# Kernel tuning notes

Hardware: AMD Instinct MI355X
Metric: run time of the kernel (lower is better)

Reference implementation:

```python
import jax, jax.numpy as jnp
import numpy as np

N = 100000      # total nodes across batch of graphs
E = 1600000     # total edges (avg degree 16)
DIN = 16        # raw node feature dim
H = 128         # social_hidden_dim
HEADS = 4
DOUT = H // HEADS
LAYERS = 2
G = 64          # number of graphs in batch
FOUT = 256      # fusion_hidden_dim
NEG_SLOPE = 0.2


def layer_norm(x, g, b, eps=1e-5):
    mu = x.mean(-1, keepdims=True)
    var = ((x - mu) ** 2).mean(-1, keepdims=True)
    return (x - mu) / jnp.sqrt(var + eps) * g + b


def gat_conv(h, src, dst, W, a_src, a_dst, bias):
    # h: [N,H]; src/dst: [E+N] (self-loops included)
    hp = (h @ W).reshape(N, HEADS, DOUT)                    # [N,heads,dout]
    al_s = jnp.einsum('nhd,hd->nh', hp, a_src)              # [N,heads]
    al_d = jnp.einsum('nhd,hd->nh', hp, a_dst)
    logits = jax.nn.leaky_relu(al_s[src] + al_d[dst], NEG_SLOPE)  # [Etot,heads]
    m = jax.ops.segment_max(logits, dst, num_segments=N)    # segment softmax over dst
    e = jnp.exp(logits - m[dst])
    denom = jax.ops.segment_sum(e, dst, num_segments=N)
    alpha = e / (denom[dst] + 1e-16)                        # [Etot,heads]
    msg = hp[src] * alpha[:, :, None]                       # [Etot,heads,dout]
    out = jax.ops.segment_sum(msg, dst, num_segments=N)     # scatter-add
    return out.reshape(N, H) + bias


def setup_inputs():
    key = jax.random.key(0)
    ks = jax.random.split(key, 24)
    s = 0.05
    inp = {
        'x': jax.random.normal(ks[0], (N, DIN), jnp.float32),
        'edge_index': jax.random.randint(ks[1], (2, E), 0, N, jnp.int32),
        'node2graph': (jnp.arange(N, dtype=jnp.int32) * G // N).astype(jnp.int32),
        'Wp': jax.random.normal(ks[2], (DIN, H)) * s,
        'bp': jnp.zeros((H,)),
        'Wq1': jax.random.normal(ks[3], (2 * H, H)) * s,
        'bq1': jnp.zeros((H,)),
        'gq': jnp.ones((H,)), 'beq': jnp.zeros((H,)),
        'Wq2': jax.random.normal(ks[4], (H, FOUT)) * s,
        'bq2': jnp.zeros((FOUT,)),
    }
    for i in range(LAYERS):
        inp[f'Wg{i}'] = jax.random.normal(ks[5 + 4 * i], (H, H)) * s
        inp[f'as{i}'] = jax.random.normal(ks[6 + 4 * i], (HEADS, DOUT)) * s
        inp[f'ad{i}'] = jax.random.normal(ks[7 + 4 * i], (HEADS, DOUT)) * s
        inp[f'bg{i}'] = jnp.zeros((H,))
        inp[f'g{i}'] = jnp.ones((H,))
        inp[f'be{i}'] = jnp.zeros((H,))
    return inp


def reference(x, edge_index, node2graph, Wp, bp, Wq1, bq1, gq, beq, Wq2, bq2,
              Wg0, as0, ad0, bg0, g0, be0, Wg1, as1, ad1, bg1, g1, be1):
    loop = jnp.arange(N, dtype=edge_index.dtype)
    src = jnp.concatenate([edge_index[0], loop])  # add self-loops (PyG default)
    dst = jnp.concatenate([edge_index[1], loop])

    h = jax.nn.gelu(x @ Wp + bp, approximate=False)
    params = [(Wg0, as0, ad0, bg0, g0, be0), (Wg1, as1, ad1, bg1, g1, be1)]
    for (W, a_s, a_d, b, g, be) in params:
        h_new = gat_conv(h, src, dst, W, a_s, a_d, b)
        h = layer_norm(h_new + h, g, be)  # dims match -> residual

    counts = jax.ops.segment_sum(jnp.ones((N, 1), h.dtype), node2graph, num_segments=G)
    mean_pool = jax.ops.segment_sum(h, node2graph, num_segments=G) / jnp.maximum(counts, 1.0)
    max_pool = jax.ops.segment_max(h, node2graph, num_segments=G)
    emb = jnp.concatenate([mean_pool, max_pool], axis=-1)  # [G, 2H]

    p = layer_norm(emb @ Wq1 + bq1, gq, beq)
    p = jax.nn.gelu(p, approximate=False)
    return p @ Wq2 + bq2  # [G, FOUT]
```

## Files before the change

kernel.cpp:

```cpp
#include <hip/hip_runtime.h>

typedef unsigned short u16;
typedef unsigned char u8;
typedef unsigned int u32;
typedef unsigned long long u64;
typedef short short8 __attribute__((ext_vector_type(8)));
typedef float f32x4 __attribute__((ext_vector_type(4)));
typedef float f32x2 __attribute__((ext_vector_type(2)));

#define NN   100000
#define EE   1600000
#define NG   64
#define WSTR 136
#define NB   98
#define BCAP 24576
#define OCAP 262144
#define EPB  4096

constexpr size_t AL256(size_t x) { return (x + 255) & ~(size_t)255; }
constexpr size_t OFF_FLAG   = 0;
constexpr size_t OFF_OCNT   = AL256(OFF_FLAG + 256);
constexpr size_t OFF_BCNT   = AL256(OFF_OCNT + 128 * 4);
constexpr size_t OFF_ROWPTR = AL256(OFF_BCNT + 128 * 4);
constexpr size_t OFF_DEG    = AL256(OFF_ROWPTR + (size_t)(NN + 1) * 4);
constexpr size_t OFF_COL    = AL256(OFF_DEG + (size_t)NN * 4);
constexpr size_t OFF_ALS    = AL256(OFF_COL + (size_t)(EE + 1024) * 4);
constexpr size_t OFF_ALD    = AL256(OFF_ALS + (size_t)NN * 4 * 4);
constexpr size_t OFF_GSUM   = AL256(OFF_ALD + (size_t)NN * 4 * 4);
constexpr size_t OFF_GKEY   = AL256(OFF_GSUM + (size_t)NG * 128 * 4);
constexpr size_t OFF_GCNT   = AL256(OFF_GKEY + (size_t)NG * 128 * 4);
constexpr size_t OFF_H      = AL256(OFF_GCNT + (size_t)NG * 4);
constexpr size_t OFF_HPB    = AL256(OFF_H + (size_t)NN * 128 * 2);
constexpr size_t OFF_EBUF   = AL256(OFF_HPB + (size_t)NN * 128 * 1);
constexpr size_t OFF_OBUF   = AL256(OFF_EBUF + (size_t)NB * BCAP * 4);
constexpr size_t WS_TOTAL   = AL256(OFF_OBUF + (size_t)OCAP * 8);

__device__ u64 g_ws[WS_TOTAL / 8];

__device__ __forceinline__ char* wsp() { return (char*)g_ws; }
#define WS_FLAG   ((int*)(wsp() + OFF_FLAG))
#define WS_OCNT   ((int*)(wsp() + OFF_OCNT))
#define WS_BCNT   ((int*)(wsp() + OFF_BCNT))
#define WS_ROWPTR ((int*)(wsp() + OFF_ROWPTR))
#define WS_DEG    ((int*)(wsp() + OFF_DEG))
#define WS_COL    ((int*)(wsp() + OFF_COL))
#define WS_ALS    ((float*)(wsp() + OFF_ALS))
#define WS_ALD    ((float*)(wsp() + OFF_ALD))
#define WS_GSUM   ((float*)(wsp() + OFF_GSUM))
#define WS_GKEY   ((u32*)(wsp() + OFF_GKEY))
#define WS_GCNT   ((int*)(wsp() + OFF_GCNT))
#define WS_H      ((u16*)(wsp() + OFF_H))
#define WS_HPB    ((u8*)(wsp() + OFF_HPB))
#define WS_EBUF   ((u32*)(wsp() + OFF_EBUF))
#define WS_OBUF   ((u64*)(wsp() + OFF_OBUF))

__device__ __forceinline__ float b2f(u16 u) { return __uint_as_float(((u32)u) << 16); }
__device__ __forceinline__ float b2f_lo(u32 u) { return __uint_as_float(u << 16); }
__device__ __forceinline__ float b2f_hi(u32 u) { return __uint_as_float(u & 0xffff0000u); }
__device__ __forceinline__ u16 f2bf(float f) {
    u32 u = __float_as_uint(f);
    return (u16)((u + 0x7fffu + ((u >> 16) & 1u)) >> 16);
}
__device__ __forceinline__ float ldf(const void* p, int i, int bf) {
    return bf ? b2f(((const u16*)p)[i]) : ((const float*)p)[i];
}
__device__ __forceinline__ int ldint(const int* p, long long i, int wide) {
    return wide ? p[i * 2] : p[(size_t)i];
}
__device__ __forceinline__ u32 fkey(float f) {
    u32 u = __float_as_uint(f);
    return (u >> 31) ? ~u : (u | 0x80000000u);
}
__device__ __forceinline__ float funkey(u32 k) {
    u32 u = (k & 0x80000000u) ? (k & 0x7fffffffu) : ~k;
    return __uint_as_float(u);
}

__global__ __launch_bounds__(256) void k_zero(const void* __restrict__ x,
                                              const int* __restrict__ ei) {
    if (blockIdx.x == 0 && threadIdx.x < 64) {
        int t = threadIdx.x;
        const u16* p = (const u16*)x;
        u16 u = p[t * 2];
        int e = (u >> 7) & 0xff;
        int ok = ((u & 0x7fffu) == 0) || (e >= 0x60 && e <= 0x9f);
        u64 m1 = __ballot(ok);
        int z = (ei[t * 2 + 1] == 0);
        u64 m2 = __ballot(z);
        if (t == 0) {
            WS_FLAG[0] = (__popcll(m1) >= 48) ? 1 : 0;
            WS_FLAG[1] = (__popcll(m2) >= 56) ? 1 : 0;
        }
    }
    if (blockIdx.x == 0 && threadIdx.x == 64) WS_FLAG[2] = 0;
    int i = blockIdx.x * 256 + threadIdx.x;
    if (i < NN) WS_DEG[i] = 0;
    if (i < NG * 128) { WS_GSUM[i] = 0.f; WS_GKEY[i] = 0u; }
    if (i < NG) WS_GCNT[i] = 0;
    if (i < NB) { WS_BCNT[i] = 0; WS_OCNT[i] = 0; }
}

__global__ __launch_bounds__(256) void k_bucket(const int* __restrict__ ei) {
    __shared__ int lcnt[NB], lbase[NB], lcur[NB];
    int t = threadIdx.x;
    int wide = WS_FLAG[1];
    for (int i = t; i < NB; i += 256) { lcnt[i] = 0; lcur[i] = 0; }
    __syncthreads();
    int e0 = blockIdx.x * EPB + t;
    int sA[16], dA[16];
#pragma unroll
    for (int j = 0; j < 16; j++) {
        int e = e0 + j * 256;
        int s = -1, d = 0;
        if (e < EE) {
            if (wide) { s = ((const int2*)ei)[e].x; d = ((const int2*)ei)[(size_t)EE + e].x; }
            else      { s = ei[e];                  d = ei[(size_t)EE + e]; }
            if ((u32)s >= NN || (u32)d >= NN) s = -1;
        }
        sA[j] = s; dA[j] = d;
        if (s >= 0) atomicAdd(&lcnt[d >> 10], 1);
    }
    __syncthreads();
    for (int i = t; i < NB; i += 256)
        lbase[i] = atomicAdd(&WS_BCNT[i], lcnt[i]);
    __syncthreads();
    u32* ebuf = WS_EBUF;
#pragma unroll
    for (int j = 0; j < 16; j++) {
        int s = sA[j], d = dA[j];
        if (s < 0) continue;
        int b = d >> 10;
        int r = atomicAdd(&lcur[b], 1);
        int slot = lbase[b] + r;
        if (slot < BCAP) {
            ebuf[(size_t)b * BCAP + slot] = ((u32)(d & 1023) << 17) | (u32)s;
        } else {
            int o = atomicAdd(&WS_FLAG[2], 1);
            if (o < OCAP) {
                WS_OBUF[o] = ((u64)(u32)d << 32) | (u32)s;
                atomicAdd(&WS_DEG[d], 1);
                atomicAdd(&WS_OCNT[d >> 10], 1);
            }
        }
    }
}

__global__ __launch_bounds__(1024) void k_place() {
    __shared__ int hist[1024];
    __shared__ int sb[128];
    __shared__ int wsum[16];
    __shared__ int w0tot;
    int b = blockIdx.x, t = threadIdx.x;
    int lane = t & 63, wv = t >> 6;
    hist[t] = 0;
    if (t < 128) {
        int c = 0;
        if (t < NB) {
            c = WS_BCNT[t]; if (c > BCAP) c = BCAP;
            c += WS_OCNT[t];
        }
        int x = c;
#pragma unroll
        for (int off = 1; off < 64; off <<= 1) {
            int y = __shfl_up(x, off);
            if (lane >= off) x += y;
        }
        if (t == 63) w0tot = x;
        sb[t] = x;
    }
    __syncthreads();
    if (t >= 64 && t < 128) sb[t] += w0tot;
    __syncthreads();
    int base = (b > 0) ? sb[b - 1] : 0;
    if (b == 0 && t == 0) WS_ROWPTR[NN] = sb[NB - 1];
    int bc = WS_BCNT[b]; if (bc > BCAP) bc = BCAP;
    const u32* eb = WS_EBUF + (size_t)b * BCAP;
    for (int i = t; i < bc; i += 1024)
        atomicAdd(&hist[eb[i] >> 17], 1);
    __syncthreads();
    int n = (b << 10) + t;
    int v = (n < NN) ? (hist[t] + WS_DEG[n]) : 0;
    int x = v;
#pragma unroll
    for (int off = 1; off < 64; off <<= 1) {
        int y = __shfl_up(x, off);
        if (lane >= off) x += y;
    }
    if (lane == 63) wsum[wv] = x;
    __syncthreads();
    if (wv == 0 && lane < 16) {
        int y = wsum[lane];
#pragma unroll
        for (int off = 1; off < 16; off <<= 1) {
            int z = __shfl_up(y, off);
            if (lane >= off) y += z;
        }
        wsum[lane] = y;
    }
    __syncthreads();
    int r = base + x + (wv > 0 ? wsum[wv - 1] : 0) - v;
    if (n < NN) WS_ROWPTR[n] = r;
    __syncthreads();
    hist[t] = r;
    __syncthreads();
    for (int i = t; i < bc; i += 1024) {
        u32 pk = eb[i];
        int pos = atomicAdd(&hist[pk >> 17], 1);
        WS_COL[pos] = (int)(pk & 0x1ffffu);
    }
    int cnt = WS_FLAG[2]; if (cnt > OCAP) cnt = OCAP;
    for (int i = t; i < cnt; i += 1024) {
        u64 pk = WS_OBUF[i];
        int d = (int)(pk >> 32);
        if ((d >> 10) == b) {
            int pos = atomicAdd(&hist[d & 1023], 1);
            WS_COL[pos] = (int)(pk & 0xffffffffu);
        }
    }
}

__global__ __launch_bounds__(128) void k_proj(const void* __restrict__ x,
                                              const void* __restrict__ Wp,
                                              const void* __restrict__ bp) {
    __shared__ float sW[16 * 128];
    int t = threadIdx.x;
    int bf = WS_FLAG[0];
    for (int i = t; i < 16 * 128; i += 128) sW[i] = ldf(Wp, i, bf);
    __syncthreads();
    float bj = ldf(bp, t, bf);
    for (int n = blockIdx.x; n < NN; n += gridDim.x) {
        float acc = bj;
#pragma unroll
        for (int k = 0; k < 16; k++)
            acc = fmaf(ldf(x, n * 16 + k, bf), sW[k * 128 + t], acc);
        float g = 0.5f * acc * (1.0f + erff(acc * 0.70710678118654752f));
        WS_H[(size_t)n * 128 + t] = f2bf(g);
    }
}

__global__ __launch_bounds__(256) void k_gemm(const void* __restrict__ Wg,
                                              const void* __restrict__ a_s,
                                              const void* __restrict__ a_d) {
    __shared__ __align__(16) u16 sWt[128 * WSTR];
    __shared__ __align__(16) u16 sH[16 * WSTR];
    int t = threadIdx.x;
    int bf = WS_FLAG[0];
    for (int idx = t; idx < 128 * 128; idx += 256) {
        int k = idx >> 7, n = idx & 127;
        sWt[n * WSTR + k] = bf ? ((const u16*)Wg)[idx] : f2bf(((const float*)Wg)[idx]);
    }
    __syncthreads();
    int wv = t >> 6, lane = t & 63;
    int n0 = wv * 32;
    int quad = lane >> 4, m16 = lane & 15;
    int ce = n0 + 2 * m16;
    float as0v = ldf(a_s, ce, bf),     as1v = ldf(a_s, ce + 1, bf);
    float ad0v = ldf(a_d, ce, bf),     ad1v = ldf(a_d, ce + 1, bf);
    short8 bfr[2][4];
#pragma unroll
    for (int nt = 0; nt < 2; nt++) {
        int n = ce + nt;
#pragma unroll
        for (int ks = 0; ks < 4; ks++)
            bfr[nt][ks] = *(const short8*)&sWt[n * WSTR + ks * 32 + quad * 8];
    }
    u8* hp = WS_HPB;
    const u32* h32 = (const u32*)WS_H;
    u32* sH32 = (u32*)sH;
    for (int m0 = blockIdx.x * 16; m0 < NN; m0 += gridDim.x * 16) {
        __syncthreads();
        for (int idx = t; idx < 16 * 64; idx += 256) {
            int r = idx >> 6, c2 = idx & 63;
            sH32[r * 68 + c2] = h32[(size_t)(m0 + r) * 64 + c2];
        }
        __syncthreads();
        f32x4 acc0 = {0.f, 0.f, 0.f, 0.f};
        f32x4 acc1 = {0.f, 0.f, 0.f, 0.f};
#pragma unroll
        for (int ks = 0; ks < 4; ks++) {
            short8 af = *(const short8*)&sH[m16 * WSTR + ks * 32 + quad * 8];
            acc0 = __builtin_amdgcn_mfma_f32_16x16x32_bf16(af, bfr[0][ks], acc0, 0, 0, 0);
            acc1 = __builtin_amdgcn_mfma_f32_16x16x32_bf16(af, bfr[1][ks], acc1, 0, 0, 0);
        }
#pragma unroll
        for (int r = 0; r < 4; r++) {
            size_t row = (size_t)(m0 + quad * 4 + r) * 128;
            u32 pk8 = (u32)__builtin_amdgcn_cvt_pk_fp8_f32(acc0[r], acc1[r], 0, false);
            *(u16*)&hp[row + ce] = (u16)(pk8 & 0xffffu);
            float ps = acc0[r] * as0v + acc1[r] * as1v;
            float pd = acc0[r] * ad0v + acc1[r] * ad1v;
#pragma unroll
            for (int m = 1; m <= 8; m <<= 1) {
                ps += __shfl_xor(ps, m);
                pd += __shfl_xor(pd, m);
            }
            if (m16 == 0) {
                int nrow = m0 + quad * 4 + r;
                WS_ALS[nrow * 4 + wv] = ps;
                WS_ALD[nrow * 4 + wv] = pd;
            }
        }
    }
}

__global__ __launch_bounds__(512) void k_gat(const void* __restrict__ bg,
                                             const void* __restrict__ gam,
                                             const void* __restrict__ bet) {
    int wid = threadIdx.x >> 6, lane = threadIdx.x & 63;
    int n = blockIdx.x * 8 + wid;
    if (n >= NN) return;
    int bf = WS_FLAG[0];
    const int* col = WS_COL;
    const float* als = WS_ALS;
    int k0 = WS_ROWPTR[n], deg = WS_ROWPTR[n + 1] - k0;
    int hd = lane >> 4, eo = lane & 15;
    float aldh = WS_ALD[n * 4 + hd];
    const u16* hp16 = (const u16*)WS_HPB;
    u32* h32 = (u32*)WS_H;
    u32 hv = h32[(size_t)n * 64 + lane];
    u16 pvs = hp16[(size_t)n * 64 + lane];
    int base48 = lane & 48;

    float vs = als[n * 4 + hd] + aldh;
    vs = vs > 0.f ? vs : 0.2f * vs;
    float wself = __expf(vs);

    int i0 = eo, i1 = eo + 16;
    int e0 = k0 + (i0 < deg ? i0 : 0);
    int e1 = k0 + (i1 < deg ? i1 : 0);
    int sc0 = col[e0];
    int sc1 = col[e1];
    if ((u32)sc0 >= NN) sc0 = 0;
    if ((u32)sc1 >= NN) sc1 = 0;
    float v0 = als[sc0 * 4 + hd] + aldh;
    float v1 = als[sc1 * 4 + hd] + aldh;
    v0 = v0 > 0.f ? v0 : 0.2f * v0;
    v1 = v1 > 0.f ? v1 : 0.2f * v1;
    float w0 = (i0 < deg) ? __expf(v0) : 0.f;
    float w1 = (i1 < deg) ? __expf(v1) : 0.f;
    float se = w0 + w1;
    f32x2 mvs = __builtin_amdgcn_cvt_pk_f32_fp8((int)pvs, false);
    float a0 = wself * mvs.x, a1 = wself * mvs.y;

#pragma unroll
    for (int j = 0; j < 16; j++) {
        float wj = __shfl(w0, base48 + j);
        int   sj = __builtin_amdgcn_readlane(sc0, j);
        u16 pv = hp16[(size_t)sj * 64 + lane];
        f32x2 mv = __builtin_amdgcn_cvt_pk_f32_fp8((int)pv, false);
        a0 = fmaf(wj, mv.x, a0);
        a1 = fmaf(wj, mv.y, a1);
    }
    if (deg > 16) {
#pragma unroll
        for (int j = 0; j < 16; j++) {
            float wj = __shfl(w1, base48 + j);
            int   sj = __builtin_amdgcn_readlane(sc1, j);
            u16 pv = hp16[(size_t)sj * 64 + lane];
            f32x2 mv = __builtin_amdgcn_cvt_pk_f32_fp8((int)pv, false);
            a0 = fmaf(wj, mv.x, a0);
            a1 = fmaf(wj, mv.y, a1);
        }
    }

    if (__builtin_expect(deg > 32, 0)) {
        for (int c = 32; c < deg; c += 16) {
            int i = c + eo;
            float w = 0.f; int scol = 0;
            if (i < deg) {
                scol = col[k0 + i];
                float v = als[scol * 4 + hd] + aldh;
                v = v > 0.f ? v : 0.2f * v;
                w = __expf(v);
            }
            se += w;
            int rem = deg - c; if (rem > 16) rem = 16;
            for (int j = 0; j < rem; j++) {
                float wj = __shfl(w, base48 + j);
                int sj = __shfl(scol, base48 + j);
                u16 pv = hp16[(size_t)sj * 64 + lane];
                f32x2 mv = __builtin_amdgcn_cvt_pk_f32_fp8((int)pv, false);
                a0 = fmaf(wj, mv.x, a0);
                a1 = fmaf(wj, mv.y, a1);
            }
        }
    }

    se += __shfl_xor(se, 1);
    se += __shfl_xor(se, 2);
    se += __shfl_xor(se, 4);
    se += __shfl_xor(se, 8);
    se += wself;
    float inv = 1.f / (se + 1e-16f);
    int d0 = lane * 2, d1 = d0 + 1;
    float r0 = a0 * inv + ldf(bg, d0, bf) + b2f_lo(hv);
    float r1 = a1 * inv + ldf(bg, d1, bf) + b2f_hi(hv);
    float s1 = r0 + r1;
#pragma unroll
    for (int m = 1; m <= 32; m <<= 1) s1 += __shfl_xor(s1, m);
    float mu = s1 * (1.f / 128.f);
    float e0f = r0 - mu, e1f = r1 - mu;
    float s2 = e0f * e0f + e1f * e1f;
#pragma unroll
    for (int m = 1; m <= 32; m <<= 1) s2 += __shfl_xor(s2, m);
    float rstd = rsqrtf(s2 * (1.f / 128.f) + 1e-5f);
    float y0 = e0f * rstd * ldf(gam, d0, bf) + ldf(bet, d0, bf);
    float y1 = e1f * rstd * ldf(gam, d1, bf) + ldf(bet, d1, bf);
    h32[(size_t)n * 64 + lane] = (u32)f2bf(y0) | ((u32)f2bf(y1) << 16);
}

__global__ __launch_bounds__(128) void k_pool(const int* __restrict__ n2g) {
    int j = threadIdx.x;
    int wide = WS_FLAG[1];
    int n0 = blockIdx.x * 128;
    int n1 = n0 + 128; if (n1 > NN) n1 = NN;
    float runs = 0.f, runm = -3.4e38f;
    int rung = -1, runc = 0;
    for (int n = n0; n < n1; n++) {
        int g = ldint(n2g, n, wide);
        if (g != rung) {
            if (rung >= 0 && (u32)rung < NG) {
                atomicAdd(&WS_GSUM[rung * 128 + j], runs);
                atomicMax(&WS_GKEY[rung * 128 + j], fkey(runm));
                if (j == 0) atomicAdd(&WS_GCNT[rung], runc);
            }
            rung = g; runs = 0.f; runm = -3.4e38f; runc = 0;
        }
        float v = b2f(WS_H[(size_t)n * 128 + j]);
        runs += v;
        runm = fmaxf(runm, v);
        runc++;
    }
    if (rung >= 0 && (u32)rung < NG) {
        atomicAdd(&WS_GSUM[rung * 128 + j], runs);
        atomicMax(&WS_GKEY[rung * 128 + j], fkey(runm));
        if (j == 0) atomicAdd(&WS_GCNT[rung], runc);
    }
}

__global__ __launch_bounds__(256) void k_head(const void* __restrict__ Wq1,
                                              const void* __restrict__ bq1,
                                              const void* __restrict__ gq,
                                              const void* __restrict__ beq,
                                              const void* __restrict__ Wq2,
                                              const void* __restrict__ bq2,
                                              float* __restrict__ out) {
    __shared__ float sem[256];
    __shared__ float sp[128];
    __shared__ float red[4];
    int g = blockIdx.x, t = threadIdx.x;
    int bf = WS_FLAG[0];
    float cnt = fmaxf((float)WS_GCNT[g], 1.f);
    if (t < 128) sem[t] = WS_GSUM[g * 128 + t] / cnt;
    else         sem[t] = funkey(WS_GKEY[g * 128 + (t - 128)]);
    __syncthreads();
    float a = 0.f;
    if (t < 128) {
        a = ldf(bq1, t, bf);
        for (int k = 0; k < 256; k++) a = fmaf(sem[k], ldf(Wq1, k * 128 + t, bf), a);
    }
    int lane = t & 63, wv = t >> 6;
    float s1 = (t < 128) ? a : 0.f;
#pragma unroll
    for (int m = 1; m <= 32; m <<= 1) s1 += __shfl_xor(s1, m);
    if (lane == 0) red[wv] = s1;
    __syncthreads();
    float mu = (red[0] + red[1]) * (1.f / 128.f);
    float d = (t < 128) ? (a - mu) : 0.f;
    float s2 = d * d;
#pragma unroll
    for (int m = 1; m <= 32; m <<= 1) s2 += __shfl_xor(s2, m);
    __syncthreads();
    if (lane == 0) red[wv] = s2;
    __syncthreads();
    float var = (red[0] + red[1]) * (1.f / 128.f);
    if (t < 128) {
        float p = d * rsqrtf(var + 1e-5f) * ldf(gq, t, bf) + ldf(beq, t, bf);
        sp[t] = 0.5f * p * (1.0f + erff(p * 0.70710678118654752f));
    }
    __syncthreads();
    float o = ldf(bq2, t, bf);
    for (int k = 0; k < 128; k++)
        o = fmaf(sp[k], ldf(Wq2, k * 256 + t, bf), o);
    out[g * 256 + t] = o;
}

extern "C" void kernel_launch(void* const* d_in, const int* in_sizes, int n_in,
                              void* d_out, int out_size, void* d_ws, size_t ws_size,
                              hipStream_t stream) {
    const void* x   = d_in[0];
    const int* ei   = (const int*)d_in[1];
    const int* n2g  = (const int*)d_in[2];
    const void* Wp  = d_in[3];
    const void* bp  = d_in[4];
    const void* Wq1 = d_in[5];
    const void* bq1 = d_in[6];
    const void* gq  = d_in[7];
    const void* beq = d_in[8];
    const void* Wq2 = d_in[9];
    const void* bq2 = d_in[10];
    const void* Wg0 = d_in[11];
    const void* as0 = d_in[12];
    const void* ad0 = d_in[13];
    const void* bg0 = d_in[14];
    const void* g0  = d_in[15];
    const void* be0 = d_in[16];
    const void* Wg1 = d_in[17];
    const void* as1 = d_in[18];
    const void* ad1 = d_in[19];
    const void* bg1 = d_in[20];
    const void* g1  = d_in[21];
    const void* be1 = d_in[22];
    (void)d_ws; (void)ws_size; (void)in_sizes; (void)n_in; (void)out_size;

    k_zero<<<(NN + 255) / 256, 256, 0, stream>>>(x, ei);

    k_bucket<<<(EE + EPB - 1) / EPB, 256, 0, stream>>>(ei);
    k_place<<<NB, 1024, 0, stream>>>();

    k_proj<<<2048, 128, 0, stream>>>(x, Wp, bp);

    k_gemm<<<1024, 256, 0, stream>>>(Wg0, as0, ad0);
    k_gat<<<(NN + 7) / 8, 512, 0, stream>>>(bg0, g0, be0);
    k_gemm<<<1024, 256, 0, stream>>>(Wg1, as1, ad1);
    k_gat<<<(NN + 7) / 8, 512, 0, stream>>>(bg1, g1, be1);

    k_pool<<<(NN + 127) / 128, 128, 0, stream>>>(n2g);
    k_head<<<NG, 256, 0, stream>>>(Wq1, bq1, gq, beq, Wq2, bq2, (float*)d_out);
}
```

Before: 519.3 us.

## Use finer CSR buckets, larger GEMM row tiles, and split-K head matmul

Edge bucketing now uses 512-node buckets (196 blocks of 512 threads) instead of 1024-node buckets, so CSR placement runs across more workgroups with smaller per-block histograms. The node-projection GEMM processes 32 rows per iteration as two 16-row MFMA sub-tiles on a 768-block grid, which amortises the shared-memory staging and barriers over more rows. The head kernel splits the 256-deep Wq1 dot product across all 256 threads and then sums the two halves. In exchange, the block-level prefix scan is more complex and the smaller bucket capacity may push more edges into the overflow path.

```diff
diff --git a/kernel.cpp b/kernel.cpp
--- a/kernel.cpp
+++ b/kernel.cpp
@@ -12,16 +12,18 @@
 #define EE   1600000
 #define NG   64
 #define WSTR 136
-#define NB   98
-#define BCAP 24576
+#define NB   196
+#define BSHIFT 9
+#define BMASK 511
+#define BCAP 12288
 #define OCAP 262144
 #define EPB  4096
 
 constexpr size_t AL256(size_t x) { return (x + 255) & ~(size_t)255; }
 constexpr size_t OFF_FLAG   = 0;
 constexpr size_t OFF_OCNT   = AL256(OFF_FLAG + 256);
-constexpr size_t OFF_BCNT   = AL256(OFF_OCNT + 128 * 4);
-constexpr size_t OFF_ROWPTR = AL256(OFF_BCNT + 128 * 4);
+constexpr size_t OFF_BCNT   = AL256(OFF_OCNT + 256 * 4);
+constexpr size_t OFF_ROWPTR = AL256(OFF_BCNT + 256 * 4);
 constexpr size_t OFF_DEG    = AL256(OFF_ROWPTR + (size_t)(NN + 1) * 4);
 constexpr size_t OFF_COL    = AL256(OFF_DEG + (size_t)NN * 4);
 constexpr size_t OFF_ALS    = AL256(OFF_COL + (size_t)(EE + 1024) * 4);
@@ -118,7 +120,7 @@
             if ((u32)s >= NN || (u32)d >= NN) s = -1;
         }
         sA[j] = s; dA[j] = d;
-        if (s >= 0) atomicAdd(&lcnt[d >> 10], 1);
+        if (s >= 0) atomicAdd(&lcnt[d >> BSHIFT], 1);
     }
     __syncthreads();
     for (int i = t; i < NB; i += 256)
@@ -129,31 +131,31 @@
     for (int j = 0; j < 16; j++) {
         int s = sA[j], d = dA[j];
         if (s < 0) continue;
-        int b = d >> 10;
+        int b = d >> BSHIFT;
         int r = atomicAdd(&lcur[b], 1);
         int slot = lbase[b] + r;
         if (slot < BCAP) {
-            ebuf[(size_t)b * BCAP + slot] = ((u32)(d & 1023) << 17) | (u32)s;
+            ebuf[(size_t)b * BCAP + slot] = ((u32)(d & BMASK) << 17) | (u32)s;
         } else {
             int o = atomicAdd(&WS_FLAG[2], 1);
             if (o < OCAP) {
                 WS_OBUF[o] = ((u64)(u32)d << 32) | (u32)s;
                 atomicAdd(&WS_DEG[d], 1);
-                atomicAdd(&WS_OCNT[d >> 10], 1);
+                atomicAdd(&WS_OCNT[d >> BSHIFT], 1);
             }
         }
     }
 }
 
-__global__ __launch_bounds__(1024) void k_place() {
-    __shared__ int hist[1024];
-    __shared__ int sb[128];
-    __shared__ int wsum[16];
-    __shared__ int w0tot;
+__global__ __launch_bounds__(512) void k_place() {
+    __shared__ int hist[512];
+    __shared__ int sbase[256];
+    __shared__ int bws[4];
+    __shared__ int wsum[8];
     int b = blockIdx.x, t = threadIdx.x;
     int lane = t & 63, wv = t >> 6;
     hist[t] = 0;
-    if (t < 128) {
+    if (t < 256) {
         int c = 0;
         if (t < NB) {
             c = WS_BCNT[t]; if (c > BCAP) c = BCAP;
@@ -165,20 +167,26 @@
             int y = __shfl_up(x, off);
             if (lane >= off) x += y;
         }
-        if (t == 63) w0tot = x;
-        sb[t] = x;
-    }
-    __syncthreads();
-    if (t >= 64 && t < 128) sb[t] += w0tot;
-    __syncthreads();
-    int base = (b > 0) ? sb[b - 1] : 0;
-    if (b == 0 && t == 0) WS_ROWPTR[NN] = sb[NB - 1];
+        if (lane == 63) bws[wv] = x;
+        sbase[t] = x;
+    }
+    __syncthreads();
+    if (t == 0) {
+        int a = 0;
+#pragma unroll
+        for (int i = 0; i < 4; i++) { int tmp = bws[i]; bws[i] = a; a += tmp; }
+    }
+    __syncthreads();
+    if (t < 256) sbase[t] += bws[t >> 6];
+    __syncthreads();
+    int base = (b > 0) ? sbase[b - 1] : 0;
+    if (b == 0 && t == 0) WS_ROWPTR[NN] = sbase[NB - 1];
     int bc = WS_BCNT[b]; if (bc > BCAP) bc = BCAP;
     const u32* eb = WS_EBUF + (size_t)b * BCAP;
-    for (int i = t; i < bc; i += 1024)
+    for (int i = t; i < bc; i += 512)
         atomicAdd(&hist[eb[i] >> 17], 1);
     __syncthreads();
-    int n = (b << 10) + t;
+    int n = (b << BSHIFT) + t;
     int v = (n < NN) ? (hist[t] + WS_DEG[n]) : 0;
     int x = v;
 #pragma unroll
@@ -188,10 +196,10 @@
     }
     if (lane == 63) wsum[wv] = x;
     __syncthreads();
-    if (wv == 0 && lane < 16) {
+    if (wv == 0 && lane < 8) {
         int y = wsum[lane];
 #pragma unroll
-        for (int off = 1; off < 16; off <<= 1) {
+        for (int off = 1; off < 8; off <<= 1) {
             int z = __shfl_up(y, off);
             if (lane >= off) y += z;
         }
@@ -203,17 +211,17 @@
     __syncthreads();
     hist[t] = r;
     __syncthreads();
-    for (int i = t; i < bc; i += 1024) {
+    for (int i = t; i < bc; i += 512) {
         u32 pk = eb[i];
         int pos = atomicAdd(&hist[pk >> 17], 1);
         WS_COL[pos] = (int)(pk & 0x1ffffu);
     }
     int cnt = WS_FLAG[2]; if (cnt > OCAP) cnt = OCAP;
-    for (int i = t; i < cnt; i += 1024) {
+    for (int i = t; i < cnt; i += 512) {
         u64 pk = WS_OBUF[i];
         int d = (int)(pk >> 32);
-        if ((d >> 10) == b) {
-            int pos = atomicAdd(&hist[d & 1023], 1);
+        if ((d >> BSHIFT) == b) {
+            int pos = atomicAdd(&hist[d & BMASK], 1);
             WS_COL[pos] = (int)(pk & 0xffffffffu);
         }
     }
@@ -242,7 +250,7 @@
                                               const void* __restrict__ a_s,
                                               const void* __restrict__ a_d) {
     __shared__ __align__(16) u16 sWt[128 * WSTR];
-    __shared__ __align__(16) u16 sH[16 * WSTR];
+    __shared__ __align__(16) u16 sH[32 * WSTR];
     int t = threadIdx.x;
     int bf = WS_FLAG[0];
     for (int idx = t; idx < 128 * 128; idx += 256) {
@@ -267,37 +275,41 @@
     u8* hp = WS_HPB;
     const u32* h32 = (const u32*)WS_H;
     u32* sH32 = (u32*)sH;
-    for (int m0 = blockIdx.x * 16; m0 < NN; m0 += gridDim.x * 16) {
+    for (int m0 = blockIdx.x * 32; m0 < NN; m0 += gridDim.x * 32) {
         __syncthreads();
-        for (int idx = t; idx < 16 * 64; idx += 256) {
+        for (int idx = t; idx < 32 * 64; idx += 256) {
             int r = idx >> 6, c2 = idx & 63;
             sH32[r * 68 + c2] = h32[(size_t)(m0 + r) * 64 + c2];
         }
         __syncthreads();
-        f32x4 acc0 = {0.f, 0.f, 0.f, 0.f};
-        f32x4 acc1 = {0.f, 0.f, 0.f, 0.f};
-#pragma unroll
-        for (int ks = 0; ks < 4; ks++) {
-            short8 af = *(const short8*)&sH[m16 * WSTR + ks * 32 + quad * 8];
-            acc0 = __builtin_amdgcn_mfma_f32_16x16x32_bf16(af, bfr[0][ks], acc0, 0, 0, 0);
-            acc1 = __builtin_amdgcn_mfma_f32_16x16x32_bf16(af, bfr[1][ks], acc1, 0, 0, 0);
-        }
-#pragma unroll
-        for (int r = 0; r < 4; r++) {
-            size_t row = (size_t)(m0 + quad * 4 + r) * 128;
-            u32 pk8 = (u32)__builtin_amdgcn_cvt_pk_fp8_f32(acc0[r], acc1[r], 0, false);
-            *(u16*)&hp[row + ce] = (u16)(pk8 & 0xffffu);
-            float ps = acc0[r] * as0v + acc1[r] * as1v;
-            float pd = acc0[r] * ad0v + acc1[r] * ad1v;
-#pragma unroll
-            for (int m = 1; m <= 8; m <<= 1) {
-                ps += __shfl_xor(ps, m);
-                pd += __shfl_xor(pd, m);
+#pragma unroll
+        for (int sub = 0; sub < 2; sub++) {
+            f32x4 acc0 = {0.f, 0.f, 0.f, 0.f};
+            f32x4 acc1 = {0.f, 0.f, 0.f, 0.f};
+#pragma unroll
+            for (int ks = 0; ks < 4; ks++) {
+                short8 af = *(const short8*)&sH[(sub * 16 + m16) * WSTR + ks * 32 + quad * 8];
+                acc0 = __builtin_amdgcn_mfma_f32_16x16x32_bf16(af, bfr[0][ks], acc0, 0, 0, 0);
+                acc1 = __builtin_amdgcn_mfma_f32_16x16x32_bf16(af, bfr[1][ks], acc1, 0, 0, 0);
             }
-            if (m16 == 0) {
-                int nrow = m0 + quad * 4 + r;
-                WS_ALS[nrow * 4 + wv] = ps;
-                WS_ALD[nrow * 4 + wv] = pd;
+            int mbase = m0 + sub * 16;
+#pragma unroll
+            for (int r = 0; r < 4; r++) {
+                size_t row = (size_t)(mbase + quad * 4 + r) * 128;
+                u32 pk8 = (u32)__builtin_amdgcn_cvt_pk_fp8_f32(acc0[r], acc1[r], 0, false);
+                *(u16*)&hp[row + ce] = (u16)(pk8 & 0xffffu);
+                float ps = acc0[r] * as0v + acc1[r] * as1v;
+                float pd = acc0[r] * ad0v + acc1[r] * ad1v;
+#pragma unroll
+                for (int m = 1; m <= 8; m <<= 1) {
+                    ps += __shfl_xor(ps, m);
+                    pd += __shfl_xor(pd, m);
+                }
+                if (m16 == 0) {
+                    int nrow = mbase + quad * 4 + r;
+                    WS_ALS[nrow * 4 + wv] = ps;
+                    WS_ALD[nrow * 4 + wv] = pd;
+                }
             }
         }
     }
@@ -446,6 +458,7 @@
                                               const void* __restrict__ bq2,
                                               float* __restrict__ out) {
     __shared__ float sem[256];
+    __shared__ float sp2[256];
     __shared__ float sp[128];
     __shared__ float red[4];
     int g = blockIdx.x, t = threadIdx.x;
@@ -454,11 +467,17 @@
     if (t < 128) sem[t] = WS_GSUM[g * 128 + t] / cnt;
     else         sem[t] = funkey(WS_GKEY[g * 128 + (t - 128)]);
     __syncthreads();
+    {
+        int half = t >> 7, o = t & 127;
+        float acc = half ? 0.f : ldf(bq1, o, bf);
+        int kb = half * 128;
+        for (int k = kb; k < kb + 128; k++)
+            acc = fmaf(sem[k], ldf(Wq1, k * 128 + o, bf), acc);
+        sp2[t] = acc;
+    }
+    __syncthreads();
     float a = 0.f;
-    if (t < 128) {
-        a = ldf(bq1, t, bf);
-        for (int k = 0; k < 256; k++) a = fmaf(sem[k], ldf(Wq1, k * 128 + t, bf), a);
-    }
+    if (t < 128) a = sp2[t] + sp2[t + 128];
     int lane = t & 63, wv = t >> 6;
     float s1 = (t < 128) ? a : 0.f;
 #pragma unroll
@@ -516,13 +535,13 @@
     k_zero<<<(NN + 255) / 256, 256, 0, stream>>>(x, ei);
 
     k_bucket<<<(EE + EPB - 1) / EPB, 256, 0, stream>>>(ei);
-    k_place<<<NB, 1024, 0, stream>>>();
+    k_place<<<NB, 512, 0, stream>>>();
 
     k_proj<<<2048, 128, 0, stream>>>(x, Wp, bp);
 
-    k_gemm<<<1024, 256, 0, stream>>>(Wg0, as0, ad0);
+    k_gemm<<<768, 256, 0, stream>>>(Wg0, as0, ad0);
     k_gat<<<(NN + 7) / 8, 512, 0, stream>>>(bg0, g0, be0);
-    k_gemm<<<1024, 256, 0, stream>>>(Wg1, as1, ad1);
+    k_gemm<<<768, 256, 0, stream>>>(Wg1, as1, ad1);
     k_gat<<<(NN + 7) / 8, 512, 0, stream>>>(bg1, g1, be1);
 
     k_pool<<<(NN + 127) / 128, 128, 0, stream>>>(n2g);
```

Result: no change. 523.8 us (+0.9%).
